# Kernel optimization log

Hardware: AMD Instinct MI355X
Metric: run time of the kernel (lower is better)

The kernel has to match this reference:

```python
import jax, jax.numpy as jnp
import numpy as np
from jax import lax

EPS = 1e-5

def _conv1d(x, w, b):
    # x: [B,C,L], w: [O,I,K], valid padding, stride 1
    y = lax.conv_general_dilated(x, w, window_strides=(1,), padding='VALID',
                                 dimension_numbers=('NCH', 'OIH', 'NCH'))
    return y + b[None, :, None]

def setup_inputs() -> dict:
    key = jax.random.key(0)
    ks = jax.random.split(key, 7)
    B, L, C = 16, 4096, 512
    x = jax.random.normal(ks[0], (B, L, C), dtype=jnp.float32)
    fan3 = 1.0 / np.sqrt(C * 3)
    fan1 = 1.0 / np.sqrt(C * 1)
    w_down = jax.random.uniform(ks[1], (C, C, 3), jnp.float32, -fan3, fan3)
    b_down = jax.random.uniform(ks[2], (C,), jnp.float32, -fan3, fan3)
    w_pad = jax.random.uniform(ks[3], (C, C, 1), jnp.float32, -fan1, fan1)
    b_pad = jax.random.uniform(ks[4], (C,), jnp.float32, -fan1, fan1)
    gamma = jnp.ones((C,), jnp.float32)
    beta = jnp.zeros((C,), jnp.float32)
    return {"x": x, "w_down": w_down, "b_down": b_down,
            "w_pad": w_pad, "b_pad": b_pad, "gamma": gamma, "beta": beta}

def reference(x, w_down, b_down, w_pad, b_pad, gamma, beta):
    # d == 2 branch of ConvLayer
    B, L, C = x.shape

    def branch(xs):  # xs: [B, L//2, C]
        xt = jnp.transpose(xs, (0, 2, 1))                 # [B,C,L/2]
        p1 = _conv1d(xt, w_down, b_down)                  # [B,C,L/2-2]
        p2 = _conv1d(xt[:, :, :2], w_pad, b_pad)          # [B,C,2]
        return jnp.concatenate([p1, p2], axis=2)          # [B,C,L/2]

    x1_p = branch(x[:, 0::2, :])
    x2_p = branch(x[:, 1::2, :])
    # interleave: even positions from x1_p, odd from x2_p
    x_p = jnp.stack([x1_p, x2_p], axis=3).reshape(B, C, L)

    # BatchNorm1d in training mode: batch stats over (batch, length)
    mean = jnp.mean(x_p, axis=(0, 2), keepdims=True)
    var = jnp.var(x_p, axis=(0, 2), keepdims=True)
    xn = (x_p - mean) * lax.rsqrt(var + EPS)
    xn = xn * gamma[None, :, None] + beta[None, :, None]

    y = jax.nn.elu(xn)                                    # dropout = identity (eval)
    y = y + jnp.transpose(x, (0, 2, 1))                   # residual [B,C,L]

    # MaxPool1d(kernel=3, stride=2, padding=1)
    yp = jnp.pad(y, ((0, 0), (0, 0), (1, 1)), constant_values=-jnp.inf)
    pooled = lax.reduce_window(yp, -jnp.inf, lax.max, (1, 1, 3), (1, 1, 2), 'VALID')
    return jnp.transpose(pooled, (0, 2, 1))               # [B, L//2, C]
```

## Files before the change

### kernel.cpp

```cpp
#include <hip/hip_runtime.h>
#include <hip/hip_bf16.h>
#include <math.h>

typedef __bf16 bf16;
typedef __bf16 bf16x8 __attribute__((ext_vector_type(8)));
typedef float floatx4 __attribute__((ext_vector_type(4)));

#define GAS __attribute__((address_space(1)))
#define LAS __attribute__((address_space(3)))

static constexpr int B_ = 16, L_ = 4096, C_ = 512;
static constexpr int M_ = B_ * L_;
static constexpr int K_ = 3 * C_;

__global__ void prep(const float* __restrict__ x, bf16* __restrict__ xb,
                     const float* __restrict__ wd, bf16* __restrict__ wr) {
    if (blockIdx.x < 16384) {
        const size_t i = ((size_t)blockIdx.x * 256 + threadIdx.x) * 8;
        floatx4 a = *(const floatx4*)(x + i);
        floatx4 b = *(const floatx4*)(x + i + 4);
        bf16x8 o;
#pragma unroll
        for (int j = 0; j < 4; ++j) { o[j] = (bf16)a[j]; o[4 + j] = (bf16)b[j]; }
        *(bf16x8*)(xb + i) = o;
    } else {
        int idx = (blockIdx.x - 16384) * 256 + threadIdx.x;
        int o   = idx / K_;
        int rem = idx - o * K_;
        int kk  = rem >> 9;
        int i   = rem & 511;
        wr[idx] = (bf16)wd[o * K_ + i * 3 + kk];
    }
}

__global__ __launch_bounds__(512, 2) void gemm_conv(
    const bf16* __restrict__ x, const bf16* __restrict__ wr,
    const float* __restrict__ bd, bf16* __restrict__ xp, float* __restrict__ sums)
{
    __shared__ bf16 As[2 * 256 * 64];
    __shared__ bf16 Bs[2 * 256 * 64];

    const int tid = threadIdx.x;
    const int u   = blockIdx.x;
    const int mb  = (u & 7) + 8 * (u >> 4);
    const int nb  = (u >> 3) & 1;
    const int m0  = mb * 256;
    const int n0  = nb * 256;

    const int wave = tid >> 6;
    const int lane = tid & 63;
    const int wm = wave & 1;
    const int wn = wave >> 1;
    const int tm = lane & 15;
    const int quad = lane >> 4;

    floatx4 acc[8][4];
#pragma unroll
    for (int i = 0; i < 8; ++i)
#pragma unroll
        for (int j = 0; j < 4; ++j) acc[i][j] = floatx4{0.f, 0.f, 0.f, 0.f};

    int srow[4], ssc[4];
#pragma unroll
    for (int j = 0; j < 4; ++j) {
        const int qa = tid + 512 * j;
        srow[j] = qa >> 3;
        ssc[j]  = (qa & 7) ^ (srow[j] & 7);
    }

    const int xo0 = (quad ^ (tm & 7)) << 3;
    const int xo1 = ((4 + quad) ^ (tm & 7)) << 3;
    int aoff[8], boff[4];
#pragma unroll
    for (int mi = 0; mi < 8; ++mi) aoff[mi] = (wm * 128 + mi * 16 + tm) * 64;
#pragma unroll
    for (int ni = 0; ni < 4; ++ni) boff[ni] = (wn * 64 + ni * 16 + tm) * 64;

    auto stage = [&](int t, int b) {
        const int kk = t >> 3;
        const int i0 = (t & 7) << 6;
        bf16* Ad = As + b * (256 * 64);
        bf16* Bd = Bs + b * (256 * 64);
#pragma unroll
        for (int j = 0; j < 4; ++j) {
            int sr = m0 + srow[j] + 2 * kk; if (sr > M_ - 1) sr = M_ - 1;
            const bf16* sa = x + (size_t)sr * C_ + i0 + ssc[j] * 8;
            __builtin_amdgcn_global_load_lds((const GAS void*)sa,
                (LAS void*)(Ad + (tid + 512 * j) * 8), 16, 0, 0);
            const bf16* sb = wr + (size_t)(n0 + srow[j]) * K_ + kk * C_ + i0 + ssc[j] * 8;
            __builtin_amdgcn_global_load_lds((const GAS void*)sb,
                (LAS void*)(Bd + (tid + 512 * j) * 8), 16, 0, 0);
        }
    };

    auto compute = [&](const bf16* Ab, const bf16* Bb) {
        bf16x8 bfr[2][4];
#pragma unroll
        for (int kh = 0; kh < 2; ++kh)
#pragma unroll
            for (int ni = 0; ni < 4; ++ni)
                bfr[kh][ni] = *(const bf16x8*)(Bb + boff[ni] + (kh ? xo1 : xo0));
#pragma unroll
        for (int mq = 0; mq < 2; ++mq) {
            bf16x8 afr[2][4];
#pragma unroll
            for (int kh = 0; kh < 2; ++kh)
#pragma unroll
                for (int mi = 0; mi < 4; ++mi)
                    afr[kh][mi] = *(const bf16x8*)(Ab + aoff[mq * 4 + mi] + (kh ? xo1 : xo0));
            __builtin_amdgcn_s_setprio(1);
#pragma unroll
            for (int kh = 0; kh < 2; ++kh)
#pragma unroll
                for (int mi = 0; mi < 4; ++mi)
#pragma unroll
                    for (int ni = 0; ni < 4; ++ni)
                        acc[mq * 4 + mi][ni] = __builtin_amdgcn_mfma_f32_16x16x32_bf16(
                            afr[kh][mi], bfr[kh][ni], acc[mq * 4 + mi][ni], 0, 0, 0);
            __builtin_amdgcn_s_setprio(0);
        }
    };

    stage(0, 0);
    stage(1, 1);
    asm volatile("s_waitcnt vmcnt(8)" ::: "memory");
    asm volatile("s_barrier" ::: "memory");

    for (int kt2 = 0; kt2 < 22; kt2 += 2) {
        compute(As, Bs);
        asm volatile("s_barrier" ::: "memory");
        stage(kt2 + 2, 0);
        asm volatile("s_waitcnt vmcnt(8)" ::: "memory");
        asm volatile("s_barrier" ::: "memory");

        compute(As + 256 * 64, Bs + 256 * 64);
        asm volatile("s_barrier" ::: "memory");
        stage(kt2 + 3, 1);
        asm volatile("s_waitcnt vmcnt(8)" ::: "memory");
        asm volatile("s_barrier" ::: "memory");
    }
    compute(As, Bs);
    asm volatile("s_barrier" ::: "memory");
    asm volatile("s_waitcnt vmcnt(0)" ::: "memory");
    asm volatile("s_barrier" ::: "memory");
    compute(As + 256 * 64, Bs + 256 * 64);

    float bias[4];
#pragma unroll
    for (int ni = 0; ni < 4; ++ni) bias[ni] = bd[n0 + wn * 64 + ni * 16 + tm];

    float s[4] = {0, 0, 0, 0}, q[4] = {0, 0, 0, 0};
#pragma unroll
    for (int mi = 0; mi < 8; ++mi) {
#pragma unroll
        for (int r = 0; r < 4; ++r) {
            const int m = m0 + wm * 128 + mi * 16 + quad * 4 + r;
            const bool valid = (m & (L_ - 1)) < L_ - 4;
            bf16* dst = xp + (size_t)m * C_ + n0 + wn * 64 + tm;
#pragma unroll
            for (int ni = 0; ni < 4; ++ni) {
                const float v = acc[mi][ni][r] + bias[ni];
                dst[ni * 16] = (bf16)v;
                if (valid) { s[ni] += v; q[ni] += v * v; }
            }
        }
    }
#pragma unroll
    for (int ni = 0; ni < 4; ++ni) {
        float sv = s[ni], qv = q[ni];
        sv += __shfl_xor(sv, 16); sv += __shfl_xor(sv, 32);
        qv += __shfl_xor(qv, 16); qv += __shfl_xor(qv, 32);
        if (quad == 0) {
            const int c = n0 + wn * 64 + ni * 16 + tm;
            atomicAdd(&sums[c], sv);
            atomicAdd(&sums[C_ + c], qv);
        }
    }
}

__global__ void fixup(const float* __restrict__ x, const float* __restrict__ wp,
                      const float* __restrict__ bp, bf16* __restrict__ xp,
                      float* __restrict__ sums)
{
    const int b = blockIdx.x >> 2;
    const int j = blockIdx.x & 3;
    __shared__ float xrow[C_];
    for (int i = threadIdx.x; i < C_; i += 256)
        xrow[i] = x[(size_t)(b * L_ + j) * C_ + i];
    __syncthreads();
    for (int c = threadIdx.x; c < C_; c += 256) {
        const float* w = wp + (size_t)c * C_;
        float acc = 0.f;
#pragma unroll 4
        for (int i = 0; i < C_; i += 4) {
            floatx4 wv = *(const floatx4*)(w + i);
#pragma unroll
            for (int u = 0; u < 4; ++u) acc += wv[u] * xrow[i + u];
        }
        const float v = acc + bp[c];
        xp[(size_t)(b * L_ + 4092 + j) * C_ + c] = (bf16)v;
        atomicAdd(&sums[c], v);
        atomicAdd(&sums[C_ + c], v * v);
    }
}

__global__ void final_pool(const bf16* __restrict__ xp, const bf16* __restrict__ xb,
                           const float* __restrict__ sums, const float* __restrict__ gamma,
                           const float* __restrict__ beta, float* __restrict__ out)
{
    const int gid = blockIdx.x * 256 + threadIdx.x;
    const int cg = gid & 63;
    const int t  = (gid >> 6) & 2047;
    const int b  = gid >> 17;
    const int c0 = cg << 3;

    float sc[8], sh[8];
    const float invn = 1.0f / 65536.0f;
#pragma unroll
    for (int j = 0; j < 8; ++j) {
        const int c = c0 + j;
        float mean = sums[c] * invn;
        float var  = sums[C_ + c] * invn - mean * mean;
        float scale = gamma[c] * rsqrtf(var + 1e-5f);
        sc[j] = scale;
        sh[j] = beta[c] - mean * scale;
    }

    float best[8];
#pragma unroll
    for (int j = 0; j < 8; ++j) best[j] = -INFINITY;

#pragma unroll
    for (int dl = -1; dl <= 1; ++dl) {
        const int l = 2 * t + dl;
        if (l < 0) continue;
        const size_t off = (size_t)(b * L_ + l) * C_ + c0;
        bf16x8 xpv = *(const bf16x8*)(xp + off);
        bf16x8 xv  = *(const bf16x8*)(xb + off);
#pragma unroll
        for (int j = 0; j < 8; ++j) {
            float z = sc[j] * (float)xpv[j] + sh[j];
            float y = (z > 0.f) ? z : (__expf(z) - 1.f);
            y += (float)xv[j];
            best[j] = fmaxf(best[j], y);
        }
    }
    floatx4 o0, o1;
#pragma unroll
    for (int j = 0; j < 4; ++j) { o0[j] = best[j]; o1[j] = best[4 + j]; }
    *(floatx4*)(out + (size_t)gid * 8) = o0;
    *(floatx4*)(out + (size_t)gid * 8 + 4) = o1;
}

extern "C" void kernel_launch(void* const* d_in, const int* in_sizes, int n_in,
                              void* d_out, int out_size, void* d_ws, size_t ws_size,
                              hipStream_t stream)
{
    const float* x      = (const float*)d_in[0];
    const float* w_down = (const float*)d_in[1];
    const float* b_down = (const float*)d_in[2];
    const float* w_pad  = (const float*)d_in[3];
    const float* b_pad  = (const float*)d_in[4];
    const float* gamma  = (const float*)d_in[5];
    const float* beta   = (const float*)d_in[6];
    float* out = (float*)d_out;

    char* ws = (char*)d_ws;
    bf16*  xb   = (bf16*)ws;
    bf16*  xp   = (bf16*)(ws + (size_t)M_ * C_ * 2);
    bf16*  wr   = (bf16*)(ws + (size_t)M_ * C_ * 4);
    float* sums = (float*)(ws + (size_t)M_ * C_ * 4 + (size_t)C_ * K_ * 2);

    hipMemsetAsync(sums, 0, 2 * C_ * sizeof(float), stream);
    prep<<<dim3(16384 + 3072), dim3(256), 0, stream>>>(x, xb, w_down, wr);
    gemm_conv<<<dim3(512), dim3(512), 0, stream>>>(xb, wr, b_down, xp, sums);
    fixup<<<dim3(64), dim3(256), 0, stream>>>(x, w_pad, b_pad, xp, sums);
    final_pool<<<dim3(8192), dim3(256), 0, stream>>>(xp, xb, sums, gamma, beta, out);
}
```

Baseline: 394.1 us.

## Restructure GEMM main loop into four-quadrant ping-pong schedule with interleaved staging

Splits each 256x256 block tile into 2x2 quadrants, so each wave owns a 64x32 sub-tile in each quadrant, and walks every K-step in four MFMA phases. Loads of A and B halves for the next stages are issued between the phases, together with LDS fragment reads. The goal is to overlap global-to-LDS traffic and LDS reads with MFMA work at finer granularity and to cut register pressure for fragments. In exchange it adds more barriers per iteration and more complex vmcnt/lgkmcnt bookkeeping, which could stall or be subtly wrong.

Result: no change. 401.0 us (+1.7%).

```diff
diff --git a/kernel.cpp b/kernel.cpp
--- a/kernel.cpp
+++ b/kernel.cpp
@@ -54,128 +54,183 @@
     const int tm = lane & 15;
     const int quad = lane >> 4;
 
-    floatx4 acc[8][4];
-#pragma unroll
-    for (int i = 0; i < 8; ++i)
-#pragma unroll
-        for (int j = 0; j < 4; ++j) acc[i][j] = floatx4{0.f, 0.f, 0.f, 0.f};
-
-    int srow[4], ssc[4];
-#pragma unroll
-    for (int j = 0; j < 4; ++j) {
-        const int qa = tid + 512 * j;
-        srow[j] = qa >> 3;
-        ssc[j]  = (qa & 7) ^ (srow[j] & 7);
-    }
+    floatx4 acc[2][4][2][2];
+#pragma unroll
+    for (int a = 0; a < 2; ++a)
+#pragma unroll
+        for (int b = 0; b < 4; ++b)
+#pragma unroll
+            for (int c = 0; c < 2; ++c)
+#pragma unroll
+                for (int d = 0; d < 2; ++d) acc[a][b][c][d] = floatx4{0.f, 0.f, 0.f, 0.f};
+
+    const int r0  = tid >> 3;
+    const int c0s = (tid & 7) ^ (r0 & 7);
+
+    auto stageA = [&](int t, int eta) {
+        if (t >= 24) return;
+        const int kk = t >> 3, i0 = (t & 7) << 6;
+        bf16* dst = As + (t & 1) * 16384 + eta * 8192 + tid * 8;
+        int sr0 = m0 + eta * 128 + r0 + 2 * kk;      if (sr0 > M_ - 1) sr0 = M_ - 1;
+        int sr1 = m0 + eta * 128 + r0 + 64 + 2 * kk; if (sr1 > M_ - 1) sr1 = M_ - 1;
+        __builtin_amdgcn_global_load_lds((const GAS void*)(x + (size_t)sr0 * C_ + i0 + c0s * 8),
+                                         (LAS void*)dst, 16, 0, 0);
+        __builtin_amdgcn_global_load_lds((const GAS void*)(x + (size_t)sr1 * C_ + i0 + c0s * 8),
+                                         (LAS void*)(dst + 4096), 16, 0, 0);
+    };
+    auto stageB = [&](int t, int eta) {
+        if (t >= 24) return;
+        const int kk = t >> 3, i0 = (t & 7) << 6;
+        bf16* dst = Bs + (t & 1) * 16384 + eta * 8192 + tid * 8;
+        const bf16* s0 = wr + (size_t)(n0 + eta * 128 + r0) * K_ + kk * C_ + i0 + c0s * 8;
+        __builtin_amdgcn_global_load_lds((const GAS void*)s0, (LAS void*)dst, 16, 0, 0);
+        __builtin_amdgcn_global_load_lds((const GAS void*)(s0 + (size_t)64 * K_),
+                                         (LAS void*)(dst + 4096), 16, 0, 0);
+    };
 
     const int xo0 = (quad ^ (tm & 7)) << 3;
     const int xo1 = ((4 + quad) ^ (tm & 7)) << 3;
-    int aoff[8], boff[4];
-#pragma unroll
-    for (int mi = 0; mi < 8; ++mi) aoff[mi] = (wm * 128 + mi * 16 + tm) * 64;
-#pragma unroll
-    for (int ni = 0; ni < 4; ++ni) boff[ni] = (wn * 64 + ni * 16 + tm) * 64;
-
-    auto stage = [&](int t, int b) {
-        const int kk = t >> 3;
-        const int i0 = (t & 7) << 6;
-        bf16* Ad = As + b * (256 * 64);
-        bf16* Bd = Bs + b * (256 * 64);
-#pragma unroll
-        for (int j = 0; j < 4; ++j) {
-            int sr = m0 + srow[j] + 2 * kk; if (sr > M_ - 1) sr = M_ - 1;
-            const bf16* sa = x + (size_t)sr * C_ + i0 + ssc[j] * 8;
-            __builtin_amdgcn_global_load_lds((const GAS void*)sa,
-                (LAS void*)(Ad + (tid + 512 * j) * 8), 16, 0, 0);
-            const bf16* sb = wr + (size_t)(n0 + srow[j]) * K_ + kk * C_ + i0 + ssc[j] * 8;
-            __builtin_amdgcn_global_load_lds((const GAS void*)sb,
-                (LAS void*)(Bd + (tid + 512 * j) * 8), 16, 0, 0);
-        }
-    };
-
-    auto compute = [&](const bf16* Ab, const bf16* Bb) {
-        bf16x8 bfr[2][4];
+
+    bf16x8 af[4][2];
+    bf16x8 bfr[2][2][2];
+
+    stageA(0, 0); stageB(0, 0); stageB(0, 1); stageA(0, 1);
+    stageA(1, 0); stageB(1, 1); stageA(1, 1);
+    asm volatile("s_waitcnt vmcnt(6)" ::: "memory");
+    asm volatile("s_barrier" ::: "memory");
+
+#pragma unroll 2
+    for (int t = 0; t < 24; ++t) {
+        const bf16* Ab = As + (t & 1) * 16384;
+        const bf16* Bb = Bs + (t & 1) * 16384;
+
+#pragma unroll
+        for (int mi = 0; mi < 4; ++mi) {
+            const bf16* p = Ab + (wm * 64 + mi * 16 + tm) * 64;
+            af[mi][0] = *(const bf16x8*)(p + xo0);
+            af[mi][1] = *(const bf16x8*)(p + xo1);
+        }
+#pragma unroll
+        for (int ni = 0; ni < 2; ++ni) {
+            const bf16* p = Bb + (wn * 32 + ni * 16 + tm) * 64;
+            bfr[0][ni][0] = *(const bf16x8*)(p + xo0);
+            bfr[0][ni][1] = *(const bf16x8*)(p + xo1);
+        }
+        stageB(t + 1, 0);
+        asm volatile("s_waitcnt lgkmcnt(8)" ::: "memory");
+        asm volatile("s_barrier" ::: "memory");
+        asm volatile("s_waitcnt lgkmcnt(0)" ::: "memory");
+        __builtin_amdgcn_s_setprio(1);
 #pragma unroll
         for (int kh = 0; kh < 2; ++kh)
 #pragma unroll
-            for (int ni = 0; ni < 4; ++ni)
-                bfr[kh][ni] = *(const bf16x8*)(Bb + boff[ni] + (kh ? xo1 : xo0));
-#pragma unroll
-        for (int mq = 0; mq < 2; ++mq) {
-            bf16x8 afr[2][4];
-#pragma unroll
-            for (int kh = 0; kh < 2; ++kh)
-#pragma unroll
-                for (int mi = 0; mi < 4; ++mi)
-                    afr[kh][mi] = *(const bf16x8*)(Ab + aoff[mq * 4 + mi] + (kh ? xo1 : xo0));
-            __builtin_amdgcn_s_setprio(1);
-#pragma unroll
-            for (int kh = 0; kh < 2; ++kh)
-#pragma unroll
-                for (int mi = 0; mi < 4; ++mi)
-#pragma unroll
-                    for (int ni = 0; ni < 4; ++ni)
-                        acc[mq * 4 + mi][ni] = __builtin_amdgcn_mfma_f32_16x16x32_bf16(
-                            afr[kh][mi], bfr[kh][ni], acc[mq * 4 + mi][ni], 0, 0, 0);
-            __builtin_amdgcn_s_setprio(0);
-        }
-    };
-
-    stage(0, 0);
-    stage(1, 1);
-    asm volatile("s_waitcnt vmcnt(8)" ::: "memory");
-    asm volatile("s_barrier" ::: "memory");
-
-    for (int kt2 = 0; kt2 < 22; kt2 += 2) {
-        compute(As, Bs);
-        asm volatile("s_barrier" ::: "memory");
-        stage(kt2 + 2, 0);
-        asm volatile("s_waitcnt vmcnt(8)" ::: "memory");
-        asm volatile("s_barrier" ::: "memory");
-
-        compute(As + 256 * 64, Bs + 256 * 64);
-        asm volatile("s_barrier" ::: "memory");
-        stage(kt2 + 3, 1);
-        asm volatile("s_waitcnt vmcnt(8)" ::: "memory");
-        asm volatile("s_barrier" ::: "memory");
-    }
-    compute(As, Bs);
-    asm volatile("s_barrier" ::: "memory");
-    asm volatile("s_waitcnt vmcnt(0)" ::: "memory");
-    asm volatile("s_barrier" ::: "memory");
-    compute(As + 256 * 64, Bs + 256 * 64);
-
-    float bias[4];
-#pragma unroll
-    for (int ni = 0; ni < 4; ++ni) bias[ni] = bd[n0 + wn * 64 + ni * 16 + tm];
-
-    float s[4] = {0, 0, 0, 0}, q[4] = {0, 0, 0, 0};
-#pragma unroll
-    for (int mi = 0; mi < 8; ++mi) {
-#pragma unroll
-        for (int r = 0; r < 4; ++r) {
-            const int m = m0 + wm * 128 + mi * 16 + quad * 4 + r;
-            const bool valid = (m & (L_ - 1)) < L_ - 4;
-            bf16* dst = xp + (size_t)m * C_ + n0 + wn * 64 + tm;
-#pragma unroll
-            for (int ni = 0; ni < 4; ++ni) {
-                const float v = acc[mi][ni][r] + bias[ni];
-                dst[ni * 16] = (bf16)v;
-                if (valid) { s[ni] += v; q[ni] += v * v; }
+            for (int mi = 0; mi < 4; ++mi)
+#pragma unroll
+                for (int ni = 0; ni < 2; ++ni)
+                    acc[0][mi][0][ni] = __builtin_amdgcn_mfma_f32_16x16x32_bf16(
+                        af[mi][kh], bfr[0][ni][kh], acc[0][mi][0][ni], 0, 0, 0);
+        __builtin_amdgcn_s_setprio(0);
+        asm volatile("s_barrier" ::: "memory");
+
+#pragma unroll
+        for (int ni = 0; ni < 2; ++ni) {
+            const bf16* p = Bb + (128 + wn * 32 + ni * 16 + tm) * 64;
+            bfr[1][ni][0] = *(const bf16x8*)(p + xo0);
+            bfr[1][ni][1] = *(const bf16x8*)(p + xo1);
+        }
+        stageA(t + 2, 0);
+        asm volatile("s_barrier" ::: "memory");
+        asm volatile("s_waitcnt lgkmcnt(0)" ::: "memory");
+        __builtin_amdgcn_s_setprio(1);
+#pragma unroll
+        for (int kh = 0; kh < 2; ++kh)
+#pragma unroll
+            for (int mi = 0; mi < 4; ++mi)
+#pragma unroll
+                for (int ni = 0; ni < 2; ++ni)
+                    acc[0][mi][1][ni] = __builtin_amdgcn_mfma_f32_16x16x32_bf16(
+                        af[mi][kh], bfr[1][ni][kh], acc[0][mi][1][ni], 0, 0, 0);
+        __builtin_amdgcn_s_setprio(0);
+        asm volatile("s_barrier" ::: "memory");
+
+#pragma unroll
+        for (int mi = 0; mi < 4; ++mi) {
+            const bf16* p = Ab + (128 + wm * 64 + mi * 16 + tm) * 64;
+            af[mi][0] = *(const bf16x8*)(p + xo0);
+            af[mi][1] = *(const bf16x8*)(p + xo1);
+        }
+        stageB(t + 2, 1);
+        asm volatile("s_barrier" ::: "memory");
+        asm volatile("s_waitcnt lgkmcnt(0)" ::: "memory");
+        __builtin_amdgcn_s_setprio(1);
+#pragma unroll
+        for (int kh = 0; kh < 2; ++kh)
+#pragma unroll
+            for (int mi = 0; mi < 4; ++mi)
+#pragma unroll
+                for (int ni = 0; ni < 2; ++ni)
+                    acc[1][mi][1][ni] = __builtin_amdgcn_mfma_f32_16x16x32_bf16(
+                        af[mi][kh], bfr[1][ni][kh], acc[1][mi][1][ni], 0, 0, 0);
+        __builtin_amdgcn_s_setprio(0);
+        asm volatile("s_barrier" ::: "memory");
+
+        stageA(t + 2, 1);
+        if (t < 22)       { asm volatile("s_waitcnt vmcnt(6)" ::: "memory"); }
+        else if (t == 22) { asm volatile("s_waitcnt vmcnt(0)" ::: "memory"); }
+        asm volatile("s_barrier" ::: "memory");
+        __builtin_amdgcn_s_setprio(1);
+#pragma unroll
+        for (int kh = 0; kh < 2; ++kh)
+#pragma unroll
+            for (int mi = 0; mi < 4; ++mi)
+#pragma unroll
+                for (int ni = 0; ni < 2; ++ni)
+                    acc[1][mi][0][ni] = __builtin_amdgcn_mfma_f32_16x16x32_bf16(
+                        af[mi][kh], bfr[0][ni][kh], acc[1][mi][0][ni], 0, 0, 0);
+        __builtin_amdgcn_s_setprio(0);
+        asm volatile("s_barrier" ::: "memory");
+    }
+
+    float bias[2][2], s[2][2], q[2][2];
+#pragma unroll
+    for (int nh = 0; nh < 2; ++nh)
+#pragma unroll
+        for (int ni = 0; ni < 2; ++ni) {
+            bias[nh][ni] = bd[n0 + nh * 128 + wn * 32 + ni * 16 + tm];
+            s[nh][ni] = 0.f; q[nh][ni] = 0.f;
+        }
+
+#pragma unroll
+    for (int mh = 0; mh < 2; ++mh)
+#pragma unroll
+        for (int mi = 0; mi < 4; ++mi)
+#pragma unroll
+            for (int r = 0; r < 4; ++r) {
+                const int m = m0 + mh * 128 + wm * 64 + mi * 16 + quad * 4 + r;
+                const bool valid = (m & (L_ - 1)) < L_ - 4;
+                bf16* dst = xp + (size_t)m * C_ + n0 + wn * 32 + tm;
+#pragma unroll
+                for (int nh = 0; nh < 2; ++nh)
+#pragma unroll
+                    for (int ni = 0; ni < 2; ++ni) {
+                        const float v = acc[mh][mi][nh][ni][r] + bias[nh][ni];
+                        dst[nh * 128 + ni * 16] = (bf16)v;
+                        if (valid) { s[nh][ni] += v; q[nh][ni] += v * v; }
+                    }
             }
-        }
-    }
-#pragma unroll
-    for (int ni = 0; ni < 4; ++ni) {
-        float sv = s[ni], qv = q[ni];
-        sv += __shfl_xor(sv, 16); sv += __shfl_xor(sv, 32);
-        qv += __shfl_xor(qv, 16); qv += __shfl_xor(qv, 32);
-        if (quad == 0) {
-            const int c = n0 + wn * 64 + ni * 16 + tm;
-            atomicAdd(&sums[c], sv);
-            atomicAdd(&sums[C_ + c], qv);
-        }
-    }
+#pragma unroll
+    for (int nh = 0; nh < 2; ++nh)
+#pragma unroll
+        for (int ni = 0; ni < 2; ++ni) {
+            float sv = s[nh][ni], qv = q[nh][ni];
+            sv += __shfl_xor(sv, 16); sv += __shfl_xor(sv, 32);
+            qv += __shfl_xor(qv, 16); qv += __shfl_xor(qv, 32);
+            if (quad == 0) {
+                const int c = n0 + nh * 128 + wn * 32 + ni * 16 + tm;
+                atomicAdd(&sums[c], sv);
+                atomicAdd(&sums[C_ + c], qv);
+            }
+        }
 }
 
 __global__ void fixup(const float* __restrict__ x, const float* __restrict__ wp,
```
